# Kernel tuning notes

Hardware: AMD Instinct MI355X
Metric: run time of the kernel (lower is better)

Reference implementation:

```python
import jax, jax.numpy as jnp
import numpy as np

N0, N1, N2 = 50000, 12500, 3125
E0, E1, E2 = 800000, 200000, 50000
NNZ = 200000          # nonzeros per interpolation matrix (~4 per fine node)
H = 128               # hidden_channels
F = 32                # feat_dim
L = 3                 # layers
DEC_W = 64            # decoder width


def setup_inputs() -> dict:
    key = jax.random.key(0)
    ks = iter(jax.random.split(key, 64))
    f32 = jnp.float32
    d = {}
    # node features per level
    d['x0'] = jax.random.normal(next(ks), (N0, 6), f32)
    d['x1'] = jax.random.normal(next(ks), (N1, 6), f32)
    d['x2'] = jax.random.normal(next(ks), (N2, 6), f32)
    # edge lists per level
    d['edge_index0'] = jax.random.randint(next(ks), (2, E0), 0, N0)
    d['edge_index1'] = jax.random.randint(next(ks), (2, E1), 0, N1)
    d['edge_index2'] = jax.random.randint(next(ks), (2, E2), 0, N2)
    # sparse interpolation matrices A1: [N0,N1], A2: [N0,N2] in COO
    d['A1_rows'] = jax.random.randint(next(ks), (NNZ,), 0, N0)
    d['A1_cols'] = jax.random.randint(next(ks), (NNZ,), 0, N1)
    d['A1_vals'] = jax.random.uniform(next(ks), (NNZ,), f32)
    d['A2_rows'] = jax.random.randint(next(ks), (NNZ,), 0, N0)
    d['A2_cols'] = jax.random.randint(next(ks), (NNZ,), 0, N2)
    d['A2_vals'] = jax.random.uniform(next(ks), (NNZ,), f32)
    # encoder params, stacked over L layers. GraphConv: lin_rel (bias) + lin_root (no bias)
    s = 0.05
    d['enc_c1_Wrel'] = jax.random.normal(next(ks), (L, 6, H), f32) * s
    d['enc_c1_brel'] = jnp.zeros((L, H), f32)
    d['enc_c1_Wroot'] = jax.random.normal(next(ks), (L, 6, H), f32) * s
    d['enc_c2_Wrel'] = jax.random.normal(next(ks), (L, H, H), f32) * s
    d['enc_c2_brel'] = jnp.zeros((L, H), f32)
    d['enc_c2_Wroot'] = jax.random.normal(next(ks), (L, H, H), f32) * s
    d['enc_lin_W'] = jax.random.normal(next(ks), (L, H, 3 * F), f32) * s
    d['enc_lin_b'] = jnp.zeros((L, 3 * F), f32)
    # decoder params (D=1, W=64, in=L*F, out=1), stacked over 3 decoders
    d['dec_W0'] = jax.random.normal(next(ks), (3, L * F, DEC_W), f32) * s
    d['dec_b0'] = jnp.zeros((3, DEC_W), f32)
    d['dec_Wout'] = jax.random.normal(next(ks), (3, DEC_W, 1), f32) * s
    d['dec_bout'] = jnp.zeros((3, 1), f32)
    return d


def _graph_conv(x, src, dst, Wrel, brel, Wroot, n):
    # PyG GraphConv: lin_rel(sum_{j->i} x_j) + lin_root(x_i)
    agg = jax.ops.segment_sum(x[src], dst, num_segments=n)
    return agg @ Wrel + brel + x @ Wroot


def reference(x0, x1, x2, edge_index0, edge_index1, edge_index2,
              A1_rows, A1_cols, A1_vals, A2_rows, A2_cols, A2_vals,
              enc_c1_Wrel, enc_c1_brel, enc_c1_Wroot,
              enc_c2_Wrel, enc_c2_brel, enc_c2_Wroot,
              enc_lin_W, enc_lin_b,
              dec_W0, dec_b0, dec_Wout, dec_bout):
    xs = (x0, x1, x2)
    eis = (edge_index0, edge_index1, edge_index2)

    def enc(i):
        x, ei = xs[i], eis[i]
        n = x.shape[0]
        src, dst = ei[0], ei[1]
        h = jax.nn.relu(_graph_conv(x, src, dst, enc_c1_Wrel[i], enc_c1_brel[i], enc_c1_Wroot[i], n))
        h = jax.nn.relu(_graph_conv(h, src, dst, enc_c2_Wrel[i], enc_c2_brel[i], enc_c2_Wroot[i], n))
        return h @ enc_lin_W[i] + enc_lin_b[i]  # [n, 3*F]

    e0 = enc(0).reshape(N0, 3, F)
    e1 = enc(1)  # [N1, 3F]
    e2 = enc(2)  # [N2, 3F]
    # sparse.mm(A, dense) as gather-scale-scatter
    i1 = jax.ops.segment_sum(A1_vals[:, None] * e1[A1_cols], A1_rows, num_segments=N0).reshape(N0, 3, F)
    i2 = jax.ops.segment_sum(A2_vals[:, None] * e2[A2_cols], A2_rows, num_segments=N0).reshape(N0, 3, F)
    interped = jnp.concatenate([e0, i1, i2], axis=2)  # [N0, 3, L*F]

    def dec(i):
        h = interped[:, i:i + 1, :]                       # [N0, 1, L*F]
        h = jax.nn.elu(h @ dec_W0[i] + dec_b0[i])         # [N0, 1, 64]
        return h @ dec_Wout[i] + dec_bout[i]              # [N0, 1, 1]

    return jnp.concatenate([dec(0), dec(1), dec(2)], axis=1)  # [N0, 3, 1]
```

## Files before the change

kernel.cpp:

```cpp
#include <hip/hip_runtime.h>
#include <math.h>

#define N0 50000
#define N1 12500
#define N2 3125
#define NNZ 200000
#define NE0 800000
#define NE1 200000
#define NE2 50000
#define NT 65625
#define SEG_TOT 165625
#define EDGE_TOT 1050000
#define ITEM_TOT 1450000
#define NBUCK 324
#define SPB 512
#define NBLK 355

typedef __attribute__((ext_vector_type(8))) short short8;
typedef __attribute__((ext_vector_type(8))) unsigned short ushort8;
typedef __attribute__((ext_vector_type(4))) float floatx4;

__device__ inline void split_bf16(float x, unsigned short& hi, unsigned short& lo) {
    unsigned xb = __float_as_uint(x);
    hi = (unsigned short)(xb >> 16);
    float hf = __uint_as_float((unsigned)hi << 16);
    lo = (unsigned short)(__float_as_uint(x - hf) >> 16);
}

__device__ inline void split8(const float* p, short8& hi, short8& lo) {
    float4 u0 = *(const float4*)p;
    float4 u1 = *(const float4*)(p + 4);
    float f[8] = {u0.x, u0.y, u0.z, u0.w, u1.x, u1.y, u1.z, u1.w};
#pragma unroll
    for (int j = 0; j < 8; j++) {
        unsigned short h, l;
        split_bf16(f[j], h, l);
        hi[j] = (short)h; lo[j] = (short)l;
    }
}


__device__ inline int item_seg(int t, const int* __restrict__ ei0,
                               const int* __restrict__ ei1, const int* __restrict__ ei2,
                               const int* __restrict__ A1r, const int* __restrict__ A2r) {
    if (t < NE0) return ei0[NE0 + t];
    if (t < NE0 + NE1) return 50000 + ei1[NE1 + (t - NE0)];
    if (t < EDGE_TOT) return 62500 + ei2[NE2 + (t - (NE0 + NE1))];
    if (t < EDGE_TOT + NNZ) return NT + A1r[t - EDGE_TOT];
    return NT + N0 + A2r[t - (EDGE_TOT + NNZ)];
}

__global__ __launch_bounds__(256) void bin_hist(const int* __restrict__ ei0,
        const int* __restrict__ ei1, const int* __restrict__ ei2,
        const int* __restrict__ A1r, const int* __restrict__ A2r,
        int* __restrict__ hist_g) {
    __shared__ int h[NBUCK];
    for (int i = threadIdx.x; i < NBUCK; i += 256) h[i] = 0;
    __syncthreads();
    int base = blockIdx.x * 4096;
#pragma unroll
    for (int q = 0; q < 16; q++) {
        int t = base + q * 256 + threadIdx.x;
        if (t < ITEM_TOT) atomicAdd(&h[item_seg(t, ei0, ei1, ei2, A1r, A2r) >> 9], 1);
    }
    __syncthreads();
    for (int i = threadIdx.x; i < NBUCK; i += 256) hist_g[i * NBLK + blockIdx.x] = h[i];
}

__global__ void bucket_tot_k(const int* __restrict__ hist_g, int* __restrict__ btot) {
    int b = blockIdx.x;
    int s = 0;
    for (int i = threadIdx.x; i < NBLK; i += 64) s += hist_g[b * NBLK + i];
#pragma unroll
    for (int o = 32; o > 0; o >>= 1) s += __shfl_down(s, o, 64);
    if (threadIdx.x == 0) btot[b] = s;
}

__global__ void hist_scan(int* __restrict__ hist_g, const int* __restrict__ btot,
                          int* __restrict__ bbase) {
    int b = blockIdx.x, lane = threadIdx.x;
    int s = 0;
    for (int j = lane; j < b; j += 64) s += btot[j];
#pragma unroll
    for (int o = 32; o > 0; o >>= 1) s += __shfl_down(s, o, 64);
    int base = __shfl(s, 0, 64);
    if (lane == 0) {
        bbase[b] = base;
        if (b == NBUCK - 1) bbase[NBUCK] = ITEM_TOT;
    }
    int v[6], ts = 0;
#pragma unroll
    for (int q = 0; q < 6; q++) {
        int i = lane * 6 + q;
        v[q] = (i < NBLK) ? hist_g[b * NBLK + i] : 0;
        ts += v[q];
    }
    int sc = ts;
#pragma unroll
    for (int o = 1; o < 64; o <<= 1) {
        int t2 = __shfl_up(sc, o, 64);
        if (lane >= o) sc += t2;
    }
    int run = base + sc - ts;
#pragma unroll
    for (int q = 0; q < 6; q++) {
        int i = lane * 6 + q;
        if (i < NBLK) hist_g[b * NBLK + i] = run;
        run += v[q];
    }
}

__global__ __launch_bounds__(256) void bin_scatter(const int* __restrict__ ei0,
        const int* __restrict__ ei1, const int* __restrict__ ei2,
        const int* __restrict__ A1r, const int* __restrict__ A1c, const float* __restrict__ A1v,
        const int* __restrict__ A2r, const int* __restrict__ A2c, const float* __restrict__ A2v,
        const int* __restrict__ hist_g, int* __restrict__ bpacked, float* __restrict__ bval) {
    __shared__ int cur[NBUCK];
    for (int i = threadIdx.x; i < NBUCK; i += 256) cur[i] = hist_g[i * NBLK + blockIdx.x];
    __syncthreads();
    int base = blockIdx.x * 4096;
#pragma unroll
    for (int q = 0; q < 16; q++) {
        int t = base + q * 256 + threadIdx.x;
        if (t >= ITEM_TOT) continue;
        int seg, pay;
        float val = 0.f;
        bool isv = false;
        if (t < NE0) { seg = ei0[NE0 + t]; pay = ei0[t]; }
        else if (t < NE0 + NE1) { int e = t - NE0; seg = 50000 + ei1[NE1 + e]; pay = ei1[e]; }
        else if (t < EDGE_TOT) { int e = t - (NE0 + NE1); seg = 62500 + ei2[NE2 + e]; pay = ei2[e]; }
        else if (t < EDGE_TOT + NNZ) { int k = t - EDGE_TOT; seg = NT + A1r[k]; pay = A1c[k]; val = A1v[k]; isv = true; }
        else { int k = t - (EDGE_TOT + NNZ); seg = NT + N0 + A2r[k]; pay = A2c[k]; val = A2v[k]; isv = true; }
        int bk = seg >> 9;
        int p = atomicAdd(&cur[bk], 1);
        bpacked[p] = ((seg - (bk << 9)) << 16) | pay;
        if (isv) bval[p] = val;
    }
}

__global__ __launch_bounds__(256) void bucket_fill(const int* __restrict__ bpacked,
        const float* __restrict__ bval, const int* __restrict__ bbase,
        int* __restrict__ offs, int* __restrict__ csrc, float* __restrict__ cval) {
    __shared__ int cnt[SPB];
    __shared__ int wsum2[4];
    int b = blockIdx.x, tid = threadIdx.x;
    int segbase = b * SPB;
    int seglim = SEG_TOT - segbase;
    if (seglim > SPB) seglim = SPB;
    int ibeg = bbase[b], iend = bbase[b + 1];
    for (int i = tid; i < SPB; i += 256) cnt[i] = 0;
    __syncthreads();
    for (int i = ibeg + tid; i < iend; i += 256)
        atomicAdd(&cnt[bpacked[i] >> 16], 1);
    __syncthreads();
    int lane = tid & 63, wid = tid >> 6;
    int v0 = cnt[tid * 2], v1 = cnt[tid * 2 + 1];
    int ts = v0 + v1, sc = ts;
#pragma unroll
    for (int o = 1; o < 64; o <<= 1) {
        int t2 = __shfl_up(sc, o, 64);
        if (lane >= o) sc += t2;
    }
    if (lane == 63) wsum2[wid] = sc;
    __syncthreads();
    int woff = 0;
    for (int w = 0; w < wid; w++) woff += wsum2[w];
    int ex = ibeg + woff + sc - ts;
    __syncthreads();
    cnt[tid * 2] = ex;
    cnt[tid * 2 + 1] = ex + v0;
    if (tid * 2 < seglim) offs[segbase + tid * 2] = ex;
    if (tid * 2 + 1 < seglim) offs[segbase + tid * 2 + 1] = ex + v0;
    if (b == NBUCK - 1 && tid == 0) offs[SEG_TOT] = ITEM_TOT;
    __syncthreads();
    for (int i = ibeg + tid; i < iend; i += 256) {
        int w2 = bpacked[i];
        int sl = w2 >> 16, pay = w2 & 0xffff;
        int p = atomicAdd(&cnt[sl], 1);
        csrc[p] = pay;
        if (segbase + sl >= NT) cval[p - EDGE_TOT] = bval[i];
    }
}


__global__ void gather6_b(const float* __restrict__ x0, const float* __restrict__ x1,
                          const float* __restrict__ x2, const int* __restrict__ offs,
                          const int* __restrict__ csrc, float* __restrict__ agg6) {
    int n = blockIdx.x * blockDim.x + threadIdx.x;
    if (n >= NT) return;
    const float* x = (n < 50000) ? x0 : (n < 62500 ? x1 : x2);
    float a0 = 0, a1 = 0, a2 = 0, a3 = 0, a4 = 0, a5 = 0;
    int b = offs[n], e = offs[n + 1];
    for (int j = b; j < e; j++) {
        const float* p = x + (size_t)csrc[j] * 6;
        a0 += p[0]; a1 += p[1]; a2 += p[2]; a3 += p[3]; a4 += p[4]; a5 += p[5];
    }
    float* o = agg6 + (size_t)n * 6;
    o[0] = a0; o[1] = a1; o[2] = a2; o[3] = a3; o[4] = a4; o[5] = a5;
}

__global__ __launch_bounds__(256) void gatherH_b(const unsigned short* __restrict__ h1hi,
                                                 const int* __restrict__ offs,
                                                 const int* __restrict__ csrc,
                                                 float* __restrict__ agg) {
    int t = blockIdx.x * blockDim.x + threadIdx.x;
    int n = t >> 5, g = t & 31;
    if (n >= NT) return;
    int nb = (n < 50000) ? 0 : (n < 62500 ? 50000 : 62500);
    float4 a = {0.f, 0.f, 0.f, 0.f};
    int b = offs[n], e = offs[n + 1];
    for (int j = b; j < e; j++) {
        uint2 u = *(const uint2*)(h1hi + (size_t)(nb + csrc[j]) * 128 + g * 4);
        a.x += __uint_as_float(u.x << 16);
        a.y += __uint_as_float(u.x & 0xffff0000u);
        a.z += __uint_as_float(u.y << 16);
        a.w += __uint_as_float(u.y & 0xffff0000u);
    }
    ((float4*)(agg + (size_t)n * 128))[g] = a;
}

__global__ __launch_bounds__(256) void interp_b(const float* __restrict__ ecat,
                                                const int* __restrict__ offs,
                                                const int* __restrict__ csrc,
                                                const float* __restrict__ cval,
                                                float* __restrict__ i1, float* __restrict__ i2) {
    int t = blockIdx.x * blockDim.x + threadIdx.x;
    int ng = t / 24, g = t % 24;
    if (ng >= 2 * N0) return;
    int a = (ng >= N0) ? 1 : 0;
    int nl = ng - a * N0;
    const float* e = ecat + (size_t)(a ? 62500 : 50000) * 96;
    float* ob = a ? i2 : i1;
    int seg = NT + ng;
    float4 s = {0.f, 0.f, 0.f, 0.f};
    int b = offs[seg], en = offs[seg + 1];
    for (int j = b; j < en; j++) {
        int c = csrc[j];
        float v = cval[j - EDGE_TOT];
        float4 w = ((const float4*)(e + (size_t)c * 96))[g];
        s.x += v * w.x; s.y += v * w.y; s.z += v * w.z; s.w += v * w.w;
    }
    ((float4*)(ob + (size_t)nl * 96))[g] = s;
}

__global__ void conv_weights(const float* __restrict__ c2Wrel, const float* __restrict__ c2Wroot,
                             const float* __restrict__ linW, const float* __restrict__ dW0,
                             unsigned short* __restrict__ c2hi, unsigned short* __restrict__ c2lo,
                             unsigned short* __restrict__ lhi, unsigned short* __restrict__ llo,
                             float* __restrict__ decWt) {
    int t = blockIdx.x * blockDim.x + threadIdx.x;
    if (t < 98304) {
        int i = t / 32768, r = t % 32768;
        int n = r / 256, k = r % 256;
        float w = (k < 128) ? c2Wrel[i * 16384 + k * 128 + n]
                            : c2Wroot[i * 16384 + (k - 128) * 128 + n];
        unsigned short hi, lo;
        split_bf16(w, hi, lo);
        c2hi[t] = hi; c2lo[t] = lo;
    } else if (t < 135168) {
        int u = t - 98304;
        int i = u / 12288, r = u % 12288;
        int n = r / 128, k = r % 128;
        unsigned short hi, lo;
        split_bf16(linW[i * 12288 + k * 96 + n], hi, lo);
        lhi[u] = hi; llo[u] = lo;
    } else if (t < 153600) {
        int u = t - 135168;
        int chn = u / 6144, r = u % 6144;
        int col = r / 96, k = r % 96;
        decWt[u] = dW0[chn * 6144 + k * 64 + col];
    }
}

__global__ __launch_bounds__(256) void conv1_b(
        const float* __restrict__ agg6, const float* __restrict__ x0,
        const float* __restrict__ x1, const float* __restrict__ x2,
        const float* __restrict__ Wrel, const float* __restrict__ Wroot,
        const float* __restrict__ brel,
        unsigned short* __restrict__ h1hi, unsigned short* __restrict__ h1lo) {
    __shared__ float As[16][65];
    __shared__ float Ws[16][64];
    int bx = blockIdx.x;
    int l, lbk;
    if (bx < 782) { l = 0; lbk = bx; }
    else if (bx < 978) { l = 1; lbk = bx - 782; }
    else { l = 2; lbk = bx - 978; }
    int nb = (l == 0) ? 0 : (l == 1 ? 50000 : 62500);
    int M = (l == 0) ? N0 : (l == 1 ? N1 : N2);
    const float* xl = (l == 0) ? x0 : (l == 1 ? x1 : x2);
    const float* A1 = agg6 + (size_t)nb * 6;
    const float* W1 = Wrel + l * 768;
    const float* W2 = Wroot + l * 768;
    const float* bias = brel + l * 128;
    int m0 = lbk * 64, n0 = blockIdx.y * 64;
    int tid = threadIdx.x;
    int tm = tid >> 4, tn = tid & 15;
    float acc[4][4] = {};
#pragma unroll
    for (int q = 0; q < 4; q++) {
        int idx = tid + q * 256;
        int row = idx >> 4, kk = idx & 15;
        int m = m0 + row;
        float v = 0.f;
        if (m < M && kk < 12)
            v = (kk < 6) ? A1[(size_t)m * 6 + kk] : xl[(size_t)m * 6 + kk - 6];
        As[kk][row] = v;
    }
#pragma unroll
    for (int q = 0; q < 4; q++) {
        int idx = tid + q * 256;
        int kk = idx >> 6, nn2 = idx & 63;
        float v = 0.f;
        if (kk < 12)
            v = (kk < 6) ? W1[kk * 128 + n0 + nn2] : W2[(kk - 6) * 128 + n0 + nn2];
        Ws[kk][nn2] = v;
    }
    __syncthreads();
#pragma unroll
    for (int k = 0; k < 12; k++) {
        float av[4], wv[4];
#pragma unroll
        for (int i = 0; i < 4; i++) av[i] = As[k][tm * 4 + i];
#pragma unroll
        for (int j = 0; j < 4; j++) wv[j] = Ws[k][tn * 4 + j];
#pragma unroll
        for (int i = 0; i < 4; i++)
#pragma unroll
            for (int j = 0; j < 4; j++) acc[i][j] += av[i] * wv[j];
    }
#pragma unroll
    for (int i = 0; i < 4; i++) {
        int m = m0 + tm * 4 + i;
        if (m >= M) continue;
        unsigned short hs[4], ls[4];
#pragma unroll
        for (int j = 0; j < 4; j++) {
            float v = fmaxf(acc[i][j] + bias[n0 + tn * 4 + j], 0.f);
            split_bf16(v, hs[j], ls[j]);
        }
        uint2 ph = {(unsigned)hs[0] | ((unsigned)hs[1] << 16),
                    (unsigned)hs[2] | ((unsigned)hs[3] << 16)};
        uint2 pl = {(unsigned)ls[0] | ((unsigned)ls[1] << 16),
                    (unsigned)ls[2] | ((unsigned)ls[3] << 16)};
        size_t off = (size_t)(nb + m) * 128 + n0 + tn * 4;
        *(uint2*)(h1hi + off) = ph;
        *(uint2*)(h1lo + off) = pl;
    }
}

__global__ __launch_bounds__(256) void conv2lin(
        const float* __restrict__ agg,
        const unsigned short* __restrict__ h1hi, const unsigned short* __restrict__ h1lo,
        const unsigned short* __restrict__ c2hi, const unsigned short* __restrict__ c2lo,
        const float* __restrict__ c2b,
        const unsigned short* __restrict__ lnhi, const unsigned short* __restrict__ lnlo,
        const float* __restrict__ lnb, float* __restrict__ ecat) {
    __shared__ unsigned short smem[25088];
    unsigned short* Ah = smem;
    unsigned short* Al = smem + 2560;
    unsigned short* Bh = smem + 5120;
    unsigned short* Bl = smem + 10240;
    unsigned short* Hh = smem;
    unsigned short* Hl = smem + 8704;
    unsigned short* B2h = smem + 17408;
    unsigned short* B2l = smem + 21248;
    const int LDA = 40;

    int bx = blockIdx.x;
    int l, lbk;
    if (bx < 782) { l = 0; lbk = bx; }
    else if (bx < 978) { l = 1; lbk = bx - 782; }
    else { l = 2; lbk = bx - 978; }
    int nb = (l == 0) ? 0 : (l == 1 ? 50000 : 62500);
    int M = (l == 0) ? N0 : (l == 1 ? N1 : N2);
    const float* A1 = agg + (size_t)nb * 128;
    const unsigned short* A2h = h1hi + (size_t)nb * 128;
    const unsigned short* A2l = h1lo + (size_t)nb * 128;
    const unsigned short* W1h = c2hi + l * 32768;
    const unsigned short* W1l = c2lo + l * 32768;
    const float* b1 = c2b + l * 128;
    const unsigned short* W2h = lnhi + l * 12288;
    const unsigned short* W2l = lnlo + l * 12288;
    const float* b2 = lnb + l * 96;
    float* C = ecat + (size_t)nb * 96;
    int m0 = lbk * 64;

    int tid = threadIdx.x;
    int lane = tid & 63, wid = tid >> 6;
    int waveM = wid & 1, waveN = wid >> 1;
    int l15 = lane & 15, quad = lane >> 4;
    int arow = tid >> 2, acol = (tid & 3) * 8;
    int brow = tid >> 1, bcol = (tid & 1) * 16;

    floatx4 acc[2][4];
#pragma unroll
    for (int i = 0; i < 2; i++)
#pragma unroll
        for (int j = 0; j < 4; j++) acc[i][j] = (floatx4){0.f, 0.f, 0.f, 0.f};

    for (int kt = 0; kt < 256; kt += 32) {
        __syncthreads();
        {
            int m = m0 + arow;
            ushort8 hv, lv;
            if (m < M) {
                int kg = kt + acol;
                if (kg < 128) {
                    const float* src = A1 + (size_t)m * 128 + kg;
                    float4 u0 = *(const float4*)src;
                    float4 u1 = *(const float4*)(src + 4);
                    float xv[8] = {u0.x, u0.y, u0.z, u0.w, u1.x, u1.y, u1.z, u1.w};
#pragma unroll
                    for (int q = 0; q < 8; q++) {
                        unsigned short h, lo2;
                        split_bf16(xv[q], h, lo2);
                        hv[q] = h; lv[q] = lo2;
                    }
                } else {
                    size_t off = (size_t)m * 128 + (kg - 128);
                    hv = *(const ushort8*)(A2h + off);
                    lv = *(const ushort8*)(A2l + off);
                }
            } else {
                hv = (ushort8)0; lv = (ushort8)0;
            }
            *(ushort8*)(&Ah[arow * LDA + acol]) = hv;
            *(ushort8*)(&Al[arow * LDA + acol]) = lv;
        }
        {
            const unsigned short* ph = W1h + (size_t)brow * 256 + kt + bcol;
            const unsigned short* pl = W1l + (size_t)brow * 256 + kt + bcol;
            *(ushort8*)(&Bh[brow * LDA + bcol]) = *(const ushort8*)ph;
            *(ushort8*)(&Bh[brow * LDA + bcol + 8]) = *(const ushort8*)(ph + 8);
            *(ushort8*)(&Bl[brow * LDA + bcol]) = *(const ushort8*)pl;
            *(ushort8*)(&Bl[brow * LDA + bcol + 8]) = *(const ushort8*)(pl + 8);
        }
        __syncthreads();
        short8 af[2][2];
#pragma unroll
        for (int mt = 0; mt < 2; mt++) {
            int r = waveM * 32 + mt * 16 + l15;
            af[mt][0] = *(const short8*)(&Ah[r * LDA + quad * 8]);
            af[mt][1] = *(const short8*)(&Al[r * LDA + quad * 8]);
        }
#pragma unroll
        for (int nt = 0; nt < 4; nt++) {
            int c = waveN * 64 + nt * 16 + l15;
            short8 bh = *(const short8*)(&Bh[c * LDA + quad * 8]);
            short8 bl = *(const short8*)(&Bl[c * LDA + quad * 8]);
#pragma unroll
            for (int mt = 0; mt < 2; mt++) {
                acc[mt][nt] = __builtin_amdgcn_mfma_f32_16x16x32_bf16(af[mt][0], bh, acc[mt][nt], 0, 0, 0);
                acc[mt][nt] = __builtin_amdgcn_mfma_f32_16x16x32_bf16(af[mt][0], bl, acc[mt][nt], 0, 0, 0);
                acc[mt][nt] = __builtin_amdgcn_mfma_f32_16x16x32_bf16(af[mt][1], bh, acc[mt][nt], 0, 0, 0);
            }
        }
    }

    __syncthreads();
    {
        float bs1[4];
#pragma unroll
        for (int nt = 0; nt < 4; nt++) bs1[nt] = b1[waveN * 64 + nt * 16 + l15];
#pragma unroll
        for (int mt = 0; mt < 2; mt++)
#pragma unroll
            for (int nt = 0; nt < 4; nt++)
#pragma unroll
                for (int r = 0; r < 4; r++) {
                    int row = waveM * 32 + mt * 16 + quad * 4 + r;
                    int col = waveN * 64 + nt * 16 + l15;
                    float v = fmaxf(acc[mt][nt][r] + bs1[nt], 0.f);
                    unsigned short h, lo2;
                    split_bf16(v, h, lo2);
                    Hh[row * 136 + col] = h;
                    Hl[row * 136 + col] = lo2;
                }
    }

    floatx4 acc2[2][3];
#pragma unroll
    for (int i = 0; i < 2; i++)
#pragma unroll
        for (int j = 0; j < 3; j++) acc2[i][j] = (floatx4){0.f, 0.f, 0.f, 0.f};

    for (int kt = 0; kt < 128; kt += 32) {
        __syncthreads();
        if (brow < 96) {
            const unsigned short* ph = W2h + (size_t)brow * 128 + kt + bcol;
            const unsigned short* pl = W2l + (size_t)brow * 128 + kt + bcol;
            *(ushort8*)(&B2h[brow * LDA + bcol]) = *(const ushort8*)ph;
            *(ushort8*)(&B2h[brow * LDA + bcol + 8]) = *(const ushort8*)(ph + 8);
            *(ushort8*)(&B2l[brow * LDA + bcol]) = *(const ushort8*)pl;
            *(ushort8*)(&B2l[brow * LDA + bcol + 8]) = *(const ushort8*)(pl + 8);
        }
        __syncthreads();
        short8 af2[2][2];
#pragma unroll
        for (int mt = 0; mt < 2; mt++) {
            int r = waveM * 32 + mt * 16 + l15;
            af2[mt][0] = *(const short8*)(&Hh[r * 136 + kt + quad * 8]);
            af2[mt][1] = *(const short8*)(&Hl[r * 136 + kt + quad * 8]);
        }
#pragma unroll
        for (int nt = 0; nt < 3; nt++) {
            int c = waveN * 48 + nt * 16 + l15;
            short8 bh = *(const short8*)(&B2h[c * LDA + quad * 8]);
            short8 bl = *(const short8*)(&B2l[c * LDA + quad * 8]);
#pragma unroll
            for (int mt = 0; mt < 2; mt++) {
                acc2[mt][nt] = __builtin_amdgcn_mfma_f32_16x16x32_bf16(af2[mt][0], bh, acc2[mt][nt], 0, 0, 0);
                acc2[mt][nt] = __builtin_amdgcn_mfma_f32_16x16x32_bf16(af2[mt][0], bl, acc2[mt][nt], 0, 0, 0);
                acc2[mt][nt] = __builtin_amdgcn_mfma_f32_16x16x32_bf16(af2[mt][1], bh, acc2[mt][nt], 0, 0, 0);
            }
        }
    }

    float bs2[3];
#pragma unroll
    for (int nt = 0; nt < 3; nt++) bs2[nt] = b2[waveN * 48 + nt * 16 + l15];
#pragma unroll
    for (int mt = 0; mt < 2; mt++)
#pragma unroll
        for (int r = 0; r < 4; r++) {
            int grow = m0 + waveM * 32 + mt * 16 + quad * 4 + r;
            if (grow >= M) continue;
#pragma unroll
            for (int nt = 0; nt < 3; nt++) {
                int col = waveN * 48 + nt * 16 + l15;
                C[(size_t)grow * 96 + col] = acc2[mt][nt][r] + bs2[nt];
            }
        }
}

__global__ __launch_bounds__(256) void decoder_mfma(
        const float* __restrict__ e0, const float* __restrict__ i1,
        const float* __restrict__ i2, const float* __restrict__ decWt,
        const float* __restrict__ b0, const float* __restrict__ Wout,
        const float* __restrict__ bout, float* __restrict__ out, int N) {
    __shared__ float As[6400];
    __shared__ float Bs[6400];
    __shared__ float red[64][2];
    __shared__ float sb0[64], sWo[64];
    int ch = blockIdx.y;
    int tid = threadIdx.x;
    int m0 = blockIdx.x * 64;

    for (int idx = tid; idx < 1536; idx += 256) {
        int col = idx / 24, k0 = (idx % 24) * 4;
        *(float4*)(&Bs[col * 100 + k0]) = *(const float4*)(decWt + ch * 6144 + col * 96 + k0);
    }
    if (tid < 64) { sb0[tid] = b0[ch * 64 + tid]; sWo[tid] = Wout[ch * 64 + tid]; }
    for (int idx = tid; idx < 1536; idx += 256) {
        int row = idx / 24, k0 = (idx % 24) * 4;
        int m = m0 + row;
        float4 v = {0.f, 0.f, 0.f, 0.f};
        if (m < N) {
            const float* base = (k0 < 32) ? e0 : (k0 < 64 ? i1 : i2);
            v = *(const float4*)(base + (size_t)m * 96 + ch * 32 + (k0 & 31));
        }
        *(float4*)(&As[row * 100 + k0]) = v;
    }
    __syncthreads();

    int lane = tid & 63, wid = tid >> 6;
    int waveM = wid & 1, waveN = wid >> 1;
    int l15 = lane & 15, quad = lane >> 4;
    floatx4 acc[2][2];
#pragma unroll
    for (int i = 0; i < 2; i++)
#pragma unroll
        for (int j = 0; j < 2; j++) acc[i][j] = (floatx4){0.f, 0.f, 0.f, 0.f};

#pragma unroll
    for (int kt = 0; kt < 96; kt += 32) {
        short8 ah[2], al[2];
#pragma unroll
        for (int mt = 0; mt < 2; mt++) {
            int r = waveM * 32 + mt * 16 + l15;
            split8(&As[r * 100 + kt + quad * 8], ah[mt], al[mt]);
        }
#pragma unroll
        for (int nt = 0; nt < 2; nt++) {
            int c = waveN * 32 + nt * 16 + l15;
            short8 bh, bl;
            split8(&Bs[c * 100 + kt + quad * 8], bh, bl);
#pragma unroll
            for (int mt = 0; mt < 2; mt++) {
                acc[mt][nt] = __builtin_amdgcn_mfma_f32_16x16x32_bf16(ah[mt], bh, acc[mt][nt], 0, 0, 0);
                acc[mt][nt] = __builtin_amdgcn_mfma_f32_16x16x32_bf16(ah[mt], bl, acc[mt][nt], 0, 0, 0);
                acc[mt][nt] = __builtin_amdgcn_mfma_f32_16x16x32_bf16(al[mt], bh, acc[mt][nt], 0, 0, 0);
            }
        }
    }

    float cb0[2], cwo[2];
#pragma unroll
    for (int nt = 0; nt < 2; nt++) {
        int col = waveN * 32 + nt * 16 + l15;
        cb0[nt] = sb0[col]; cwo[nt] = sWo[col];
    }
    float p[2][4];
#pragma unroll
    for (int mt = 0; mt < 2; mt++)
#pragma unroll
        for (int r = 0; r < 4; r++) {
            float s = 0.f;
#pragma unroll
            for (int nt = 0; nt < 2; nt++) {
                float h = acc[mt][nt][r] + cb0[nt];
                h = h > 0.f ? h : (expf(h) - 1.0f);
                s += h * cwo[nt];
            }
            p[mt][r] = s;
        }
#pragma unroll
    for (int mt = 0; mt < 2; mt++)
#pragma unroll
        for (int r = 0; r < 4; r++) {
#pragma unroll
            for (int msk = 1; msk < 16; msk <<= 1)
                p[mt][r] += __shfl_xor(p[mt][r], msk, 64);
        }
    if (l15 == 0) {
#pragma unroll
        for (int mt = 0; mt < 2; mt++)
#pragma unroll
            for (int r = 0; r < 4; r++) {
                int row = waveM * 32 + mt * 16 + quad * 4 + r;
                red[row][waveN] = p[mt][r];
            }
    }
    __syncthreads();
    if (tid < 64) {
        int m = m0 + tid;
        if (m < N) out[(size_t)m * 3 + ch] = red[tid][0] + red[tid][1] + bout[ch];
    }
}


extern "C" void kernel_launch(void* const* d_in, const int* in_sizes, int n_in,
                              void* d_out, int out_size, void* d_ws, size_t ws_size,
                              hipStream_t stream) {
    const float* x0 = (const float*)d_in[0];
    const float* x1 = (const float*)d_in[1];
    const float* x2 = (const float*)d_in[2];
    const int* ei0 = (const int*)d_in[3];
    const int* ei1 = (const int*)d_in[4];
    const int* ei2 = (const int*)d_in[5];
    const int* A1r = (const int*)d_in[6];
    const int* A1c = (const int*)d_in[7];
    const float* A1v = (const float*)d_in[8];
    const int* A2r = (const int*)d_in[9];
    const int* A2c = (const int*)d_in[10];
    const float* A2v = (const float*)d_in[11];
    const float* c1Wrel = (const float*)d_in[12];
    const float* c1brel = (const float*)d_in[13];
    const float* c1Wroot = (const float*)d_in[14];
    const float* c2Wrel = (const float*)d_in[15];
    const float* c2brel = (const float*)d_in[16];
    const float* c2Wroot = (const float*)d_in[17];
    const float* linW = (const float*)d_in[18];
    const float* linb = (const float*)d_in[19];
    const float* dW0 = (const float*)d_in[20];
    const float* db0 = (const float*)d_in[21];
    const float* dWout = (const float*)d_in[22];
    const float* dbout = (const float*)d_in[23];
    float* out = (float*)d_out;

    float* ws = (float*)d_ws;
    float* agg6 = ws;
    unsigned short* h1hi = (unsigned short*)(ws + 400000);
    unsigned short* h1lo = (unsigned short*)(ws + 4600000);
    float* aggH = ws + 8800000;
    float* ecat = ws + 17200000;
    float* i1 = aggH;
    float* i2 = ws + 400000;
    int* bpacked = (int*)(ws + 8800000);
    float* bval = ws + 8800000 + 1450000;
    int* hist_g = (int*)(ws + 23500000);
    int* btot = (int*)(ws + 23615020);
    int* bbase = (int*)(ws + 23615344);
    int* offs = (int*)(ws + 23665632);
    int* csrc = (int*)(ws + 23831264);
    float* cval = ws + 25281392;
    unsigned short* c2hi = (unsigned short*)(ws + 25681392);
    unsigned short* c2lo = c2hi + 98304;
    unsigned short* lnhi = c2lo + 98304;
    unsigned short* lnlo = lnhi + 36864;
    float* decWt = ws + 25681392 + 135168;

    conv_weights<<<(153600 + 255) / 256, 256, 0, stream>>>(
        c2Wrel, c2Wroot, linW, dW0, c2hi, c2lo, lnhi, lnlo, decWt);

    bin_hist<<<NBLK, 256, 0, stream>>>(ei0, ei1, ei2, A1r, A2r, hist_g);
    bucket_tot_k<<<NBUCK, 64, 0, stream>>>(hist_g, btot);
    hist_scan<<<NBUCK, 64, 0, stream>>>(hist_g, btot, bbase);
    bin_scatter<<<NBLK, 256, 0, stream>>>(ei0, ei1, ei2, A1r, A1c, A1v,
                                          A2r, A2c, A2v, hist_g, bpacked, bval);
    bucket_fill<<<NBUCK, 256, 0, stream>>>(bpacked, bval, bbase, offs, csrc, cval);

    gather6_b<<<(NT + 255) / 256, 256, 0, stream>>>(x0, x1, x2, offs, csrc, agg6);
    dim3 g1(1027, 2);
    conv1_b<<<g1, 256, 0, stream>>>(agg6, x0, x1, x2, c1Wrel, c1Wroot, c1brel, h1hi, h1lo);
    gatherH_b<<<((size_t)NT * 32 + 255) / 256, 256, 0, stream>>>(h1hi, offs, csrc, aggH);
    conv2lin<<<1027, 256, 0, stream>>>(aggH, h1hi, h1lo, c2hi, c2lo, c2brel,
                                       lnhi, lnlo, linb, ecat);

    interp_b<<<((size_t)2 * N0 * 24 + 255) / 256, 256, 0, stream>>>(
        ecat, offs, csrc, cval, i1, i2);

    dim3 gd(782, 3);
    decoder_mfma<<<gd, 256, 0, stream>>>(ecat, i1, i2, decWt, db0, dWout, dbout, out, N0);
}
```

Measured before the change: 337.6 us.

## Store hidden features in four 32-channel planes to localize gather traffic

Changes the layout of h1 (hi/lo bf16) and the aggregated hidden features from row-major [node][128] to four feature planes of [plane][node][32]. The neighbor gather kernel now launches one grid slice per plane with 16 threads per node. Each slice touches a 2 MB plane instead of the full 8 MB table, which should improve cache hit rates on the random neighbor reads. In exchange, each edge's offsets and indices are read four times, and conv1 and conv2lin must use the plane-strided addressing.

```diff
diff --git a/kernel.cpp b/kernel.cpp
--- a/kernel.cpp
+++ b/kernel.cpp
@@ -15,6 +15,7 @@
 #define NBUCK 324
 #define SPB 512
 #define NBLK 355
+#define NPB 4102
 
 typedef __attribute__((ext_vector_type(8))) short short8;
 typedef __attribute__((ext_vector_type(8))) unsigned short ushort8;
@@ -203,20 +204,22 @@
                                                  const int* __restrict__ offs,
                                                  const int* __restrict__ csrc,
                                                  float* __restrict__ agg) {
-    int t = blockIdx.x * blockDim.x + threadIdx.x;
-    int n = t >> 5, g = t & 31;
+    int bx = blockIdx.x;
+    int p = bx / NPB;
+    int tl = (bx - p * NPB) * 256 + threadIdx.x;
+    int n = tl >> 4, g = tl & 15;
     if (n >= NT) return;
     int nb = (n < 50000) ? 0 : (n < 62500 ? 50000 : 62500);
-    float4 a = {0.f, 0.f, 0.f, 0.f};
+    const unsigned short* plane = h1hi + (size_t)p * NT * 32;
+    float ax = 0.f, ay = 0.f;
     int b = offs[n], e = offs[n + 1];
     for (int j = b; j < e; j++) {
-        uint2 u = *(const uint2*)(h1hi + (size_t)(nb + csrc[j]) * 128 + g * 4);
-        a.x += __uint_as_float(u.x << 16);
-        a.y += __uint_as_float(u.x & 0xffff0000u);
-        a.z += __uint_as_float(u.y << 16);
-        a.w += __uint_as_float(u.y & 0xffff0000u);
-    }
-    ((float4*)(agg + (size_t)n * 128))[g] = a;
+        unsigned u = *(const unsigned*)(plane + (size_t)(nb + csrc[j]) * 32 + g * 2);
+        ax += __uint_as_float(u << 16);
+        ay += __uint_as_float(u & 0xffff0000u);
+    }
+    float2 a = {ax, ay};
+    *(float2*)(agg + ((size_t)p * NT + n) * 32 + g * 2) = a;
 }
 
 __global__ __launch_bounds__(256) void interp_b(const float* __restrict__ ecat,
@@ -342,14 +345,15 @@
                     (unsigned)hs[2] | ((unsigned)hs[3] << 16)};
         uint2 pl = {(unsigned)ls[0] | ((unsigned)ls[1] << 16),
                     (unsigned)ls[2] | ((unsigned)ls[3] << 16)};
-        size_t off = (size_t)(nb + m) * 128 + n0 + tn * 4;
+        int f0 = n0 + tn * 4;
+        size_t off = ((size_t)(f0 >> 5) * NT + (nb + m)) * 32 + (f0 & 31);
         *(uint2*)(h1hi + off) = ph;
         *(uint2*)(h1lo + off) = pl;
     }
 }
 
 __global__ __launch_bounds__(256) void conv2lin(
-        const float* __restrict__ agg,
+        const float* __restrict__ aggp,
         const unsigned short* __restrict__ h1hi, const unsigned short* __restrict__ h1lo,
         const unsigned short* __restrict__ c2hi, const unsigned short* __restrict__ c2lo,
         const float* __restrict__ c2b,
@@ -373,9 +377,6 @@
     else { l = 2; lbk = bx - 978; }
     int nb = (l == 0) ? 0 : (l == 1 ? 50000 : 62500);
     int M = (l == 0) ? N0 : (l == 1 ? N1 : N2);
-    const float* A1 = agg + (size_t)nb * 128;
-    const unsigned short* A2h = h1hi + (size_t)nb * 128;
-    const unsigned short* A2l = h1lo + (size_t)nb * 128;
     const unsigned short* W1h = c2hi + l * 32768;
     const unsigned short* W1l = c2lo + l * 32768;
     const float* b1 = c2b + l * 128;
@@ -405,8 +406,9 @@
             ushort8 hv, lv;
             if (m < M) {
                 int kg = kt + acol;
+                int gnode = nb + m;
                 if (kg < 128) {
-                    const float* src = A1 + (size_t)m * 128 + kg;
+                    const float* src = aggp + ((size_t)(kg >> 5) * NT + gnode) * 32 + (kg & 31);
                     float4 u0 = *(const float4*)src;
                     float4 u1 = *(const float4*)(src + 4);
                     float xv[8] = {u0.x, u0.y, u0.z, u0.w, u1.x, u1.y, u1.z, u1.w};
@@ -417,9 +419,10 @@
                         hv[q] = h; lv[q] = lo2;
                     }
                 } else {
-                    size_t off = (size_t)m * 128 + (kg - 128);
-                    hv = *(const ushort8*)(A2h + off);
-                    lv = *(const ushort8*)(A2l + off);
+                    int kp = kg - 128;
+                    size_t off = ((size_t)(kp >> 5) * NT + gnode) * 32 + (kp & 31);
+                    hv = *(const ushort8*)(h1hi + off);
+                    lv = *(const ushort8*)(h1lo + off);
                 }
             } else {
                 hv = (ushort8)0; lv = (ushort8)0;
@@ -672,9 +675,9 @@
     float* agg6 = ws;
     unsigned short* h1hi = (unsigned short*)(ws + 400000);
     unsigned short* h1lo = (unsigned short*)(ws + 4600000);
-    float* aggH = ws + 8800000;
+    float* aggp = ws + 8800000;
     float* ecat = ws + 17200000;
-    float* i1 = aggH;
+    float* i1 = aggp;
     float* i2 = ws + 400000;
     int* bpacked = (int*)(ws + 8800000);
     float* bval = ws + 8800000 + 1450000;
@@ -703,8 +706,8 @@
     gather6_b<<<(NT + 255) / 256, 256, 0, stream>>>(x0, x1, x2, offs, csrc, agg6);
     dim3 g1(1027, 2);
     conv1_b<<<g1, 256, 0, stream>>>(agg6, x0, x1, x2, c1Wrel, c1Wroot, c1brel, h1hi, h1lo);
-    gatherH_b<<<((size_t)NT * 32 + 255) / 256, 256, 0, stream>>>(h1hi, offs, csrc, aggH);
-    conv2lin<<<1027, 256, 0, stream>>>(aggH, h1hi, h1lo, c2hi, c2lo, c2brel,
+    gatherH_b<<<4 * NPB, 256, 0, stream>>>(h1hi, offs, csrc, aggp);
+    conv2lin<<<1027, 256, 0, stream>>>(aggp, h1hi, h1lo, c2hi, c2lo, c2brel,
                                        lnhi, lnlo, linb, ecat);
 
     interp_b<<<((size_t)2 * N0 * 24 + 255) / 256, 256, 0, stream>>>(
```

Result: slower. 380.7 us (+12.8%).

## Fuse sparse interpolation into decoder tile load and widen gatherH loads

Applied to the files above, without the earlier changes.

The separate interp_b kernel is removed. Each decoder block now computes its slice of the A1/A2 sparse-matrix products directly into shared memory, which avoids writing and re-reading the i1/i2 intermediates and saves one launch. In exchange, each of the three decoder channel blocks gathers only its own 32-column slice, so the per-row CSR offsets and indices are read three times. Separately, gatherH_b now uses 16 threads per node, each loading 16 bytes, and unrolls the edge loop by two to raise memory-level parallelism.

```diff
diff --git a/kernel.cpp b/kernel.cpp
--- a/kernel.cpp
+++ b/kernel.cpp
@@ -199,48 +199,42 @@
     o[0] = a0; o[1] = a1; o[2] = a2; o[3] = a3; o[4] = a4; o[5] = a5;
 }
 
+__device__ inline void acc_u4(uint4 u, float* a) {
+    a[0] += __uint_as_float(u.x << 16);
+    a[1] += __uint_as_float(u.x & 0xffff0000u);
+    a[2] += __uint_as_float(u.y << 16);
+    a[3] += __uint_as_float(u.y & 0xffff0000u);
+    a[4] += __uint_as_float(u.z << 16);
+    a[5] += __uint_as_float(u.z & 0xffff0000u);
+    a[6] += __uint_as_float(u.w << 16);
+    a[7] += __uint_as_float(u.w & 0xffff0000u);
+}
+
 __global__ __launch_bounds__(256) void gatherH_b(const unsigned short* __restrict__ h1hi,
                                                  const int* __restrict__ offs,
                                                  const int* __restrict__ csrc,
                                                  float* __restrict__ agg) {
     int t = blockIdx.x * blockDim.x + threadIdx.x;
-    int n = t >> 5, g = t & 31;
+    int n = t >> 4, g = t & 15;
     if (n >= NT) return;
     int nb = (n < 50000) ? 0 : (n < 62500 ? 50000 : 62500);
-    float4 a = {0.f, 0.f, 0.f, 0.f};
+    float a[8] = {};
     int b = offs[n], e = offs[n + 1];
-    for (int j = b; j < e; j++) {
-        uint2 u = *(const uint2*)(h1hi + (size_t)(nb + csrc[j]) * 128 + g * 4);
-        a.x += __uint_as_float(u.x << 16);
-        a.y += __uint_as_float(u.x & 0xffff0000u);
-        a.z += __uint_as_float(u.y << 16);
-        a.w += __uint_as_float(u.y & 0xffff0000u);
-    }
-    ((float4*)(agg + (size_t)n * 128))[g] = a;
-}
-
-__global__ __launch_bounds__(256) void interp_b(const float* __restrict__ ecat,
-                                                const int* __restrict__ offs,
-                                                const int* __restrict__ csrc,
-                                                const float* __restrict__ cval,
-                                                float* __restrict__ i1, float* __restrict__ i2) {
-    int t = blockIdx.x * blockDim.x + threadIdx.x;
-    int ng = t / 24, g = t % 24;
-    if (ng >= 2 * N0) return;
-    int a = (ng >= N0) ? 1 : 0;
-    int nl = ng - a * N0;
-    const float* e = ecat + (size_t)(a ? 62500 : 50000) * 96;
-    float* ob = a ? i2 : i1;
-    int seg = NT + ng;
-    float4 s = {0.f, 0.f, 0.f, 0.f};
-    int b = offs[seg], en = offs[seg + 1];
-    for (int j = b; j < en; j++) {
-        int c = csrc[j];
-        float v = cval[j - EDGE_TOT];
-        float4 w = ((const float4*)(e + (size_t)c * 96))[g];
-        s.x += v * w.x; s.y += v * w.y; s.z += v * w.z; s.w += v * w.w;
-    }
-    ((float4*)(ob + (size_t)nl * 96))[g] = s;
+    int j = b;
+    for (; j + 1 < e; j += 2) {
+        int s0 = csrc[j], s1 = csrc[j + 1];
+        uint4 u0 = *(const uint4*)(h1hi + (size_t)(nb + s0) * 128 + g * 8);
+        uint4 u1 = *(const uint4*)(h1hi + (size_t)(nb + s1) * 128 + g * 8);
+        acc_u4(u0, a);
+        acc_u4(u1, a);
+    }
+    if (j < e) {
+        uint4 u0 = *(const uint4*)(h1hi + (size_t)(nb + csrc[j]) * 128 + g * 8);
+        acc_u4(u0, a);
+    }
+    float* o = agg + (size_t)n * 128 + g * 8;
+    *(float4*)o = (float4){a[0], a[1], a[2], a[3]};
+    *(float4*)(o + 4) = (float4){a[4], a[5], a[6], a[7]};
 }
 
 __global__ void conv_weights(const float* __restrict__ c2Wrel, const float* __restrict__ c2Wroot,
@@ -534,8 +528,9 @@
 }
 
 __global__ __launch_bounds__(256) void decoder_mfma(
-        const float* __restrict__ e0, const float* __restrict__ i1,
-        const float* __restrict__ i2, const float* __restrict__ decWt,
+        const float* __restrict__ ecat, const int* __restrict__ offs,
+        const int* __restrict__ csrc, const float* __restrict__ cval,
+        const float* __restrict__ decWt,
         const float* __restrict__ b0, const float* __restrict__ Wout,
         const float* __restrict__ bout, float* __restrict__ out, int N) {
     __shared__ float As[6400];
@@ -551,15 +546,31 @@
         *(float4*)(&Bs[col * 100 + k0]) = *(const float4*)(decWt + ch * 6144 + col * 96 + k0);
     }
     if (tid < 64) { sb0[tid] = b0[ch * 64 + tid]; sWo[tid] = Wout[ch * 64 + tid]; }
-    for (int idx = tid; idx < 1536; idx += 256) {
-        int row = idx / 24, k0 = (idx % 24) * 4;
+    for (int idx = tid; idx < 512; idx += 256) {
+        int row = idx >> 3, q = idx & 7;
         int m = m0 + row;
         float4 v = {0.f, 0.f, 0.f, 0.f};
+        if (m < N) v = *(const float4*)(ecat + (size_t)m * 96 + ch * 32 + q * 4);
+        *(float4*)(&As[row * 100 + q * 4]) = v;
+    }
+    for (int idx = tid; idx < 1024; idx += 256) {
+        int row = idx >> 4;
+        int r = idx & 15;
+        int p = r >> 3, q = r & 7;
+        int m = m0 + row;
+        float4 s = {0.f, 0.f, 0.f, 0.f};
         if (m < N) {
-            const float* base = (k0 < 32) ? e0 : (k0 < 64 ? i1 : i2);
-            v = *(const float4*)(base + (size_t)m * 96 + ch * 32 + (k0 & 31));
-        }
-        *(float4*)(&As[row * 100 + k0]) = v;
+            int seg = NT + p * N0 + m;
+            const float* ebase = ecat + (size_t)(p ? 62500 : 50000) * 96 + ch * 32 + q * 4;
+            int jb = offs[seg], je = offs[seg + 1];
+            for (int j = jb; j < je; j++) {
+                int c = csrc[j];
+                float v = cval[j - EDGE_TOT];
+                float4 w = *(const float4*)(ebase + (size_t)c * 96);
+                s.x += v * w.x; s.y += v * w.y; s.z += v * w.z; s.w += v * w.w;
+            }
+        }
+        *(float4*)(&As[row * 100 + 32 + p * 32 + q * 4]) = s;
     }
     __syncthreads();
 
@@ -600,7 +611,7 @@
         int col = waveN * 32 + nt * 16 + l15;
         cb0[nt] = sb0[col]; cwo[nt] = sWo[col];
     }
-    float p[2][4];
+    float p2[2][4];
 #pragma unroll
     for (int mt = 0; mt < 2; mt++)
 #pragma unroll
@@ -612,7 +623,7 @@
                 h = h > 0.f ? h : (expf(h) - 1.0f);
                 s += h * cwo[nt];
             }
-            p[mt][r] = s;
+            p2[mt][r] = s;
         }
 #pragma unroll
     for (int mt = 0; mt < 2; mt++)
@@ -620,7 +631,7 @@
         for (int r = 0; r < 4; r++) {
 #pragma unroll
             for (int msk = 1; msk < 16; msk <<= 1)
-                p[mt][r] += __shfl_xor(p[mt][r], msk, 64);
+                p2[mt][r] += __shfl_xor(p2[mt][r], msk, 64);
         }
     if (l15 == 0) {
 #pragma unroll
@@ -628,7 +639,7 @@
 #pragma unroll
             for (int r = 0; r < 4; r++) {
                 int row = waveM * 32 + mt * 16 + quad * 4 + r;
-                red[row][waveN] = p[mt][r];
+                red[row][waveN] = p2[mt][r];
             }
     }
     __syncthreads();
@@ -674,8 +685,6 @@
     unsigned short* h1lo = (unsigned short*)(ws + 4600000);
     float* aggH = ws + 8800000;
     float* ecat = ws + 17200000;
-    float* i1 = aggH;
-    float* i2 = ws + 400000;
     int* bpacked = (int*)(ws + 8800000);
     float* bval = ws + 8800000 + 1450000;
     int* hist_g = (int*)(ws + 23500000);
@@ -703,13 +712,11 @@
     gather6_b<<<(NT + 255) / 256, 256, 0, stream>>>(x0, x1, x2, offs, csrc, agg6);
     dim3 g1(1027, 2);
     conv1_b<<<g1, 256, 0, stream>>>(agg6, x0, x1, x2, c1Wrel, c1Wroot, c1brel, h1hi, h1lo);
-    gatherH_b<<<((size_t)NT * 32 + 255) / 256, 256, 0, stream>>>(h1hi, offs, csrc, aggH);
+    gatherH_b<<<((size_t)NT * 16 + 255) / 256, 256, 0, stream>>>(h1hi, offs, csrc, aggH);
     conv2lin<<<1027, 256, 0, stream>>>(aggH, h1hi, h1lo, c2hi, c2lo, c2brel,
                                        lnhi, lnlo, linb, ecat);
 
-    interp_b<<<((size_t)2 * N0 * 24 + 255) / 256, 256, 0, stream>>>(
-        ecat, offs, csrc, cval, i1, i2);
-
     dim3 gd(782, 3);
-    decoder_mfma<<<gd, 256, 0, stream>>>(ecat, i1, i2, decWt, db0, dWout, dbout, out, N0);
-}
+    decoder_mfma<<<gd, 256, 0, stream>>>(ecat, offs, csrc, cval, decWt,
+                                         db0, dWout, dbout, out, N0);
+}
```

After: 343.1 us. No clear change (+1.6%).

## Fuse layer-2 neighbor aggregation into conv2lin GEMM kernel via shared memory

Applied to the files above, without the earlier changes.

Removes the separate gatherH_b kernel and the 128-wide fp32 aggregate written to global memory. Each conv2lin block now gathers and sums the bf16 neighbor features for its 64 rows into a padded shared-memory tile, using 16-byte loads with a two-way unrolled edge loop, and then feeds the GEMM from that tile. This saves one launch and a large global write and read. In exchange, shared memory per block grows, which may lower occupancy, and the irregular gather now runs inside the GEMM blocks before the MFMA loop starts.

```diff
diff --git a/kernel.cpp b/kernel.cpp
--- a/kernel.cpp
+++ b/kernel.cpp
@@ -199,24 +199,15 @@
     o[0] = a0; o[1] = a1; o[2] = a2; o[3] = a3; o[4] = a4; o[5] = a5;
 }
 
-__global__ __launch_bounds__(256) void gatherH_b(const unsigned short* __restrict__ h1hi,
-                                                 const int* __restrict__ offs,
-                                                 const int* __restrict__ csrc,
-                                                 float* __restrict__ agg) {
-    int t = blockIdx.x * blockDim.x + threadIdx.x;
-    int n = t >> 5, g = t & 31;
-    if (n >= NT) return;
-    int nb = (n < 50000) ? 0 : (n < 62500 ? 50000 : 62500);
-    float4 a = {0.f, 0.f, 0.f, 0.f};
-    int b = offs[n], e = offs[n + 1];
-    for (int j = b; j < e; j++) {
-        uint2 u = *(const uint2*)(h1hi + (size_t)(nb + csrc[j]) * 128 + g * 4);
-        a.x += __uint_as_float(u.x << 16);
-        a.y += __uint_as_float(u.x & 0xffff0000u);
-        a.z += __uint_as_float(u.y << 16);
-        a.w += __uint_as_float(u.y & 0xffff0000u);
-    }
-    ((float4*)(agg + (size_t)n * 128))[g] = a;
+__device__ inline void acc_u4(uint4 u, float* a) {
+    a[0] += __uint_as_float(u.x << 16);
+    a[1] += __uint_as_float(u.x & 0xffff0000u);
+    a[2] += __uint_as_float(u.y << 16);
+    a[3] += __uint_as_float(u.y & 0xffff0000u);
+    a[4] += __uint_as_float(u.z << 16);
+    a[5] += __uint_as_float(u.z & 0xffff0000u);
+    a[6] += __uint_as_float(u.w << 16);
+    a[7] += __uint_as_float(u.w & 0xffff0000u);
 }
 
 __global__ __launch_bounds__(256) void interp_b(const float* __restrict__ ecat,
@@ -349,17 +340,18 @@
 }
 
 __global__ __launch_bounds__(256) void conv2lin(
-        const float* __restrict__ agg,
         const unsigned short* __restrict__ h1hi, const unsigned short* __restrict__ h1lo,
+        const int* __restrict__ offs, const int* __restrict__ csrc,
         const unsigned short* __restrict__ c2hi, const unsigned short* __restrict__ c2lo,
         const float* __restrict__ c2b,
         const unsigned short* __restrict__ lnhi, const unsigned short* __restrict__ lnlo,
         const float* __restrict__ lnb, float* __restrict__ ecat) {
-    __shared__ unsigned short smem[25088];
-    unsigned short* Ah = smem;
-    unsigned short* Al = smem + 2560;
-    unsigned short* Bh = smem + 5120;
-    unsigned short* Bl = smem + 10240;
+    __shared__ unsigned short smem[32256];
+    float* aggT = (float*)smem;
+    unsigned short* Ah = smem + 16896;
+    unsigned short* Al = smem + 19456;
+    unsigned short* Bh = smem + 22016;
+    unsigned short* Bl = smem + 27136;
     unsigned short* Hh = smem;
     unsigned short* Hl = smem + 8704;
     unsigned short* B2h = smem + 17408;
@@ -373,7 +365,6 @@
     else { l = 2; lbk = bx - 978; }
     int nb = (l == 0) ? 0 : (l == 1 ? 50000 : 62500);
     int M = (l == 0) ? N0 : (l == 1 ? N1 : N2);
-    const float* A1 = agg + (size_t)nb * 128;
     const unsigned short* A2h = h1hi + (size_t)nb * 128;
     const unsigned short* A2l = h1lo + (size_t)nb * 128;
     const unsigned short* W1h = c2hi + l * 32768;
@@ -392,6 +383,33 @@
     int arow = tid >> 2, acol = (tid & 3) * 8;
     int brow = tid >> 1, bcol = (tid & 1) * 16;
 
+#pragma unroll
+    for (int it = 0; it < 4; it++) {
+        int slot = it * 256 + tid;
+        int node = slot >> 4, q = slot & 15;
+        int m = m0 + node;
+        float a[8] = {};
+        if (m < M) {
+            int seg = nb + m;
+            int jb = offs[seg], je = offs[seg + 1];
+            int j = jb;
+            for (; j + 1 < je; j += 2) {
+                int s0 = csrc[j], s1 = csrc[j + 1];
+                uint4 u0 = *(const uint4*)(A2h + (size_t)s0 * 128 + q * 8);
+                uint4 u1 = *(const uint4*)(A2h + (size_t)s1 * 128 + q * 8);
+                acc_u4(u0, a);
+                acc_u4(u1, a);
+            }
+            if (j < je) {
+                uint4 u0 = *(const uint4*)(A2h + (size_t)csrc[j] * 128 + q * 8);
+                acc_u4(u0, a);
+            }
+        }
+        float* o = aggT + node * 132 + q * 8;
+        *(float4*)o = (float4){a[0], a[1], a[2], a[3]};
+        *(float4*)(o + 4) = (float4){a[4], a[5], a[6], a[7]};
+    }
+
     floatx4 acc[2][4];
 #pragma unroll
     for (int i = 0; i < 2; i++)
@@ -403,24 +421,22 @@
         {
             int m = m0 + arow;
             ushort8 hv, lv;
-            if (m < M) {
-                int kg = kt + acol;
-                if (kg < 128) {
-                    const float* src = A1 + (size_t)m * 128 + kg;
-                    float4 u0 = *(const float4*)src;
-                    float4 u1 = *(const float4*)(src + 4);
-                    float xv[8] = {u0.x, u0.y, u0.z, u0.w, u1.x, u1.y, u1.z, u1.w};
-#pragma unroll
-                    for (int q = 0; q < 8; q++) {
-                        unsigned short h, lo2;
-                        split_bf16(xv[q], h, lo2);
-                        hv[q] = h; lv[q] = lo2;
-                    }
-                } else {
-                    size_t off = (size_t)m * 128 + (kg - 128);
-                    hv = *(const ushort8*)(A2h + off);
-                    lv = *(const ushort8*)(A2l + off);
+            int kg = kt + acol;
+            if (kg < 128) {
+                const float* src = aggT + arow * 132 + kg;
+                float4 u0 = *(const float4*)src;
+                float4 u1 = *(const float4*)(src + 4);
+                float xv[8] = {u0.x, u0.y, u0.z, u0.w, u1.x, u1.y, u1.z, u1.w};
+#pragma unroll
+                for (int q = 0; q < 8; q++) {
+                    unsigned short h, lo2;
+                    split_bf16(xv[q], h, lo2);
+                    hv[q] = h; lv[q] = lo2;
                 }
+            } else if (m < M) {
+                size_t off = (size_t)m * 128 + (kg - 128);
+                hv = *(const ushort8*)(A2h + off);
+                lv = *(const ushort8*)(A2l + off);
             } else {
                 hv = (ushort8)0; lv = (ushort8)0;
             }
@@ -672,12 +688,11 @@
     float* agg6 = ws;
     unsigned short* h1hi = (unsigned short*)(ws + 400000);
     unsigned short* h1lo = (unsigned short*)(ws + 4600000);
-    float* aggH = ws + 8800000;
     float* ecat = ws + 17200000;
-    float* i1 = aggH;
-    float* i2 = ws + 400000;
     int* bpacked = (int*)(ws + 8800000);
     float* bval = ws + 8800000 + 1450000;
+    float* i1 = ws + 8800000;
+    float* i2 = ws + 400000;
     int* hist_g = (int*)(ws + 23500000);
     int* btot = (int*)(ws + 23615020);
     int* bbase = (int*)(ws + 23615344);
@@ -703,8 +718,7 @@
     gather6_b<<<(NT + 255) / 256, 256, 0, stream>>>(x0, x1, x2, offs, csrc, agg6);
     dim3 g1(1027, 2);
     conv1_b<<<g1, 256, 0, stream>>>(agg6, x0, x1, x2, c1Wrel, c1Wroot, c1brel, h1hi, h1lo);
-    gatherH_b<<<((size_t)NT * 32 + 255) / 256, 256, 0, stream>>>(h1hi, offs, csrc, aggH);
-    conv2lin<<<1027, 256, 0, stream>>>(aggH, h1hi, h1lo, c2hi, c2lo, c2brel,
+    conv2lin<<<1027, 256, 0, stream>>>(h1hi, h1lo, offs, csrc, c2hi, c2lo, c2brel,
                                        lnhi, lnlo, linb, ecat);
 
     interp_b<<<((size_t)2 * N0 * 24 + 255) / 256, 256, 0, stream>>>(
```

After: 365.5 us. +8.3%, slower.
